# Performance work log

Hardware: AMD Instinct MI355X
Metric: run time of the kernel (lower is better)

## Reference

```python
import jax, jax.numpy as jnp
import numpy as np

B, S, D, H = 32, 2048, 512, 512

def setup_inputs() -> dict:
    key = jax.random.key(0)
    kx, kq, kk, kv = jax.random.split(key, 4)
    scale = 1.0 / np.sqrt(D)
    x = jax.random.normal(kx, (B, S, D), dtype=jnp.float32)
    Wq = jax.random.normal(kq, (D, H), dtype=jnp.float32) * scale
    Wk = jax.random.normal(kk, (D, H), dtype=jnp.float32) * scale
    Wv = jax.random.normal(kv, (D, H), dtype=jnp.float32) * scale
    return {"x": x, "Wq": Wq, "Wk": Wk, "Wv": Wv}

def reference(x, Wq, Wk, Wv):
    # Linear projections (bias=False)
    q = jnp.einsum('bsd,dh->bsh', x, Wq)
    k = jnp.einsum('bsd,dh->bsh', x, Wk)
    v = jnp.einsum('bsd,dh->bsh', x, Wv)
    # Pairwise KL(p_i || q_j) with p = softmax(q_i), q = softmax(k_j):
    #   KL = sum_h p_i log p_i  -  sum_h p_i log q_j
    # The first term is a per-row negative entropy; the second is a GEMM,
    # avoiding the original O(S^2) Python double loop.
    logp = jax.nn.log_softmax(q, axis=-1)          # [B,S,H]
    p = jnp.exp(logp)
    logq = jax.nn.log_softmax(k, axis=-1)          # [B,S,H]
    neg_ent = jnp.sum(p * logp, axis=-1)           # [B,S]
    cross = jnp.einsum('bih,bjh->bij', p, logq)    # [B,S,S]
    kl_divs = neg_ent[:, :, None] - cross          # [B,S,S]
    attn_weights = jax.nn.softmax(-kl_divs, axis=-1)
    attn_output = jnp.einsum('bij,bjh->bih', attn_weights, v)
    return attn_output
```

## Files before the change

kernel.cpp:

```cpp
#include <hip/hip_runtime.h>
#include <hip/hip_bf16.h>

typedef __bf16 bf16x8 __attribute__((ext_vector_type(8)));
typedef float  f32x4  __attribute__((ext_vector_type(4)));

#define NB 32
#define NS 2048
#define ND 512
#define NH 512
#define NROWS (NB*NS)
#define L2E 1.44269504f

__device__ __forceinline__ void gload16(const void* g, void* l) {
  __builtin_amdgcn_global_load_lds((const __attribute__((address_space(1))) void*)g,
                                   (__attribute__((address_space(3))) void*)l, 16, 0, 0);
}

__global__ void prep_w(const float* __restrict__ Wq, const float* __restrict__ Wk,
                       const float* __restrict__ Wv, __bf16* __restrict__ wT) {
  int i = blockIdx.x * blockDim.x + threadIdx.x;
  const int total = 3 * ND * NH;
  for (; i < total; i += gridDim.x * blockDim.x) {
    int m = i / (ND * NH);
    int rem = i - m * (ND * NH);
    int h = rem >> 9;
    int d = rem & 511;
    const float* W = (m == 0) ? Wq : ((m == 1) ? Wk : Wv);
    wT[i] = (__bf16)W[(size_t)d * NH + h];
  }
}

#define K1_XOFF 0
#define K1_WOFF 65536
#define K1_REDM 131072
#define K1_REDS 132096
#define K1_LDS  133120

__global__ __launch_bounds__(512, 2)
void proj_kernel(const float* __restrict__ x, const __bf16* __restrict__ wT,
                 __bf16* __restrict__ p_out, __bf16* __restrict__ k_out,
                 float* __restrict__ L_out, __bf16* __restrict__ vt_out)
{
  __shared__ __align__(16) char smem[K1_LDS];
  char* xb = smem + K1_XOFF;
  char* wb = smem + K1_WOFF;
  float* redm = (float*)(smem + K1_REDM);
  float* reds = (float*)(smem + K1_REDS);

  const int tid = threadIdx.x;
  const int lane = tid & 63, l15 = lane & 15, g = lane >> 4;
  const int w = tid >> 6, rt = w & 1, cs = w >> 1;
  const int r0 = blockIdx.x * 64;
  const int b = r0 >> 11, s0 = r0 & (NS - 1);

  {
    int row = tid >> 3, sc = tid & 7;
    const float* xr = x + (size_t)(r0 + row) * ND;
    #pragma unroll
    for (int u = 0; u < 8; ++u) {
      int s = u * 8 + sc;
      float4 v0 = *(const float4*)(xr + s * 8);
      float4 v1 = *(const float4*)(xr + s * 8 + 4);
      bf16x8 cv;
      cv[0]=(__bf16)v0.x; cv[1]=(__bf16)v0.y; cv[2]=(__bf16)v0.z; cv[3]=(__bf16)v0.w;
      cv[4]=(__bf16)v1.x; cv[5]=(__bf16)v1.y; cv[6]=(__bf16)v1.z; cv[7]=(__bf16)v1.w;
      *(bf16x8*)(xb + row * 1024 + ((s ^ (row & 7)) * 16)) = cv;
    }
  }
  {
    #pragma unroll
    for (int u = 0; u < 4; ++u) {
      int sid = u * 512 + tid, h = sid >> 2, gg = sid & 3;
      gload16(wT + (size_t)h * ND + ((gg ^ ((h >> 1) & 3)) * 8), wb + sid * 16);
    }
  }
  __syncthreads();

  for (int m = 0; m < 3; ++m) {
    f32x4 acc[2][8];
    #pragma unroll
    for (int i2 = 0; i2 < 2; ++i2)
      #pragma unroll
      for (int ht = 0; ht < 8; ++ht) acc[i2][ht] = (f32x4){0.f,0.f,0.f,0.f};

    for (int step = 0; step < 16; ++step) {
      int gs = m * 16 + step;
      char* wcur = wb + (gs & 1) * 32768;
      if (gs + 1 < 48) {
        int gn = gs + 1, mn = gn >> 4, sn = gn & 15;
        const __bf16* wsrc = wT + (size_t)mn * (ND * NH) + sn * 32;
        char* wdst = wb + (gn & 1) * 32768;
        #pragma unroll
        for (int u = 0; u < 4; ++u) {
          int sid = u * 512 + tid, h = sid >> 2, gg = sid & 3;
          gload16(wsrc + (size_t)h * ND + ((gg ^ ((h >> 1) & 3)) * 8), wdst + sid * 16);
        }
      }
      bf16x8 a0, a1;
      {
        int ar = rt * 32 + l15;
        a0 = *(const bf16x8*)(xb + ar * 1024 + (((step * 4 + g) ^ (ar & 7)) * 16));
        ar += 16;
        a1 = *(const bf16x8*)(xb + ar * 1024 + (((step * 4 + g) ^ (ar & 7)) * 16));
      }
      #pragma unroll
      for (int ht = 0; ht < 8; ++ht) {
        int h = cs * 128 + ht * 16 + l15;
        bf16x8 bb = *(const bf16x8*)(wcur + h * 64 + ((g ^ ((h >> 1) & 3)) * 16));
        acc[0][ht] = __builtin_amdgcn_mfma_f32_16x16x32_bf16(a0, bb, acc[0][ht], 0, 0, 0);
        acc[1][ht] = __builtin_amdgcn_mfma_f32_16x16x32_bf16(a1, bb, acc[1][ht], 0, 0, 0);
      }
      __syncthreads();
    }

    if (m == 2) {
      #pragma unroll
      for (int i2 = 0; i2 < 2; ++i2) {
        int sgg = (s0 >> 3) + rt * 4 + i2 * 2 + (g >> 1);
        size_t basep = ((size_t)(b * 256 + sgg)) * 512;
        #pragma unroll
        for (int ht = 0; ht < 8; ++ht) {
          int h = cs * 128 + ht * 16 + l15;
          union { __bf16 h4[4]; ushort4 u4; } cv;
          #pragma unroll
          for (int r = 0; r < 4; ++r) cv.h4[r] = (__bf16)acc[i2][ht][r];
          *(ushort4*)(vt_out + (basep + h) * 8 + (g & 1) * 4) = cv.u4;
        }
      }
    } else {
      float mrow[2][4], tsum[2][4];
      #pragma unroll
      for (int i2 = 0; i2 < 2; ++i2)
        #pragma unroll
        for (int r = 0; r < 4; ++r) {
          float v = acc[i2][0][r];
          #pragma unroll
          for (int ht = 1; ht < 8; ++ht) v = fmaxf(v, acc[i2][ht][r]);
          v = fmaxf(v, __shfl_xor(v, 1)); v = fmaxf(v, __shfl_xor(v, 2));
          v = fmaxf(v, __shfl_xor(v, 4)); v = fmaxf(v, __shfl_xor(v, 8));
          if (l15 == 0) redm[cs * 64 + rt * 32 + i2 * 16 + g * 4 + r] = v;
        }
      __syncthreads();
      #pragma unroll
      for (int i2 = 0; i2 < 2; ++i2)
        #pragma unroll
        for (int r = 0; r < 4; ++r) {
          int row = rt * 32 + i2 * 16 + g * 4 + r;
          mrow[i2][r] = fmaxf(fmaxf(redm[row], redm[64 + row]),
                              fmaxf(redm[128 + row], redm[192 + row]));
        }
      #pragma unroll
      for (int i2 = 0; i2 < 2; ++i2)
        #pragma unroll
        for (int r = 0; r < 4; ++r) {
          float s = 0.f;
          #pragma unroll
          for (int ht = 0; ht < 8; ++ht) s += exp2f((acc[i2][ht][r] - mrow[i2][r]) * L2E);
          s += __shfl_xor(s, 1); s += __shfl_xor(s, 2);
          s += __shfl_xor(s, 4); s += __shfl_xor(s, 8);
          if (l15 == 0) reds[cs * 64 + rt * 32 + i2 * 16 + g * 4 + r] = s;
        }
      __syncthreads();
      #pragma unroll
      for (int i2 = 0; i2 < 2; ++i2)
        #pragma unroll
        for (int r = 0; r < 4; ++r) {
          int row = rt * 32 + i2 * 16 + g * 4 + r;
          tsum[i2][r] = reds[row] + reds[64 + row] + reds[128 + row] + reds[192 + row];
        }
      __bf16* dst = (m == 0) ? p_out : k_out;
      if (m == 0) {
        #pragma unroll
        for (int i2 = 0; i2 < 2; ++i2) {
          float inv[4];
          #pragma unroll
          for (int r = 0; r < 4; ++r) inv[r] = 1.f / tsum[i2][r];
          #pragma unroll
          for (int ht = 0; ht < 8; ++ht) {
            int col = cs * 128 + ht * 16 + l15;
            #pragma unroll
            for (int r = 0; r < 4; ++r) {
              int row = rt * 32 + i2 * 16 + g * 4 + r;
              dst[(size_t)(r0 + row) * NH + col] =
                  (__bf16)(exp2f((acc[i2][ht][r] - mrow[i2][r]) * L2E) * inv[r]);
            }
          }
        }
      } else {
        #pragma unroll
        for (int i2 = 0; i2 < 2; ++i2)
          #pragma unroll
          for (int ht = 0; ht < 8; ++ht) {
            int col = cs * 128 + ht * 16 + l15;
            #pragma unroll
            for (int r = 0; r < 4; ++r) {
              int row = rt * 32 + i2 * 16 + g * 4 + r;
              dst[(size_t)(r0 + row) * NH + col] = (__bf16)acc[i2][ht][r];
            }
          }
        if (cs == 0 && l15 == 0) {
          #pragma unroll
          for (int i2 = 0; i2 < 2; ++i2)
            #pragma unroll
            for (int r = 0; r < 4; ++r) {
              int row = rt * 32 + i2 * 16 + g * 4 + r;
              L_out[r0 + row] = mrow[i2][r] + __logf(tsum[i2][r]);
            }
        }
      }
      __syncthreads();
    }
  }
}

#define QOFF 0
#define KOFF 65536
#define PSTR 512
#define A_LDS 163840

__global__ __launch_bounds__(512, 2)
void attn_kernel(const __bf16* __restrict__ p_all, const __bf16* __restrict__ k_all,
                 const float* __restrict__ L_all, const __bf16* __restrict__ vt_all,
                 float* __restrict__ out)
{
  __shared__ __align__(16) char smem[A_LDS];
  char* Qb = smem + QOFF;
  float* lred = (float*)(smem + KOFF);

  const int bid = blockIdx.x;
  const int b = ((bid >> 8) << 3) + (bid & 7);
  const int ib = (bid >> 3) & 31;
  const int i0 = ib * 64;

  const __bf16* Pg = p_all + (size_t)b * NS * NH;
  const __bf16* Kg = k_all + (size_t)b * NS * NH;
  const float*  Lg = L_all + (size_t)b * NS;
  const __bf16* Vg = vt_all + (size_t)b * (256 * 512 * 8);
  float* Og = out + ((size_t)b * NS + i0) * NH;

  const int tid = threadIdx.x;
  const int lane = tid & 63, l15 = lane & 15, g = lane >> 4;
  const int w = tid >> 6;
  const int ig = w >> 2, jg = w & 3;
  const int hs = w * 64;
  const int xr = l15 & 7;

  #define STAGE(SS) { \
    int j0_ = ((SS) >> 3) * 256, kh_ = (SS) & 7; \
    char* kd_ = smem + KOFF + ((SS) % 3) * 32768; \
    _Pragma("unroll") \
    for (int u_ = 0; u_ < 4; ++u_) { \
      int sid_ = u_ * 512 + tid, jj_ = sid_ >> 3, s8_ = sid_ & 7; \
      gload16(Kg + (size_t)(j0_ + jj_) * NH + kh_ * 64 + ((s8_ ^ (jj_ & 7)) * 8), \
              kd_ + sid_ * 16); \
    } }

  #pragma unroll
  for (int u = 0; u < 8; ++u) {
    int sid = u * 512 + tid, row = sid >> 6, s = sid & 63;
    int sp = (s & 56) | ((s ^ row) & 7);
    gload16(Pg + (size_t)(i0 + row) * NH + sp * 8, Qb + sid * 16);
  }
  STAGE(0);
  STAGE(1);

  f32x4 o_[4][4];
  #pragma unroll
  for (int it = 0; it < 4; ++it)
    #pragma unroll
    for (int ht = 0; ht < 4; ++ht) o_[it][ht] = (f32x4){0.f,0.f,0.f,0.f};
  float lsum[2][4] = {{0.f,0.f,0.f,0.f},{0.f,0.f,0.f,0.f}};

  #define LOADV(DST, JKS) { \
    _Pragma("unroll") \
    for (int ht_ = 0; ht_ < 4; ++ht_) { \
      int h_ = hs + ht_ * 16 + l15; \
      int sg_ = outer * 32 + (JKS) * 4 + g; \
      (DST)[ht_] = *(const bf16x8*)(Vg + ((size_t)sg_ * 512 + h_) * 8); \
    } }
  #define PVSTEP(JKS, VF) { \
    __builtin_amdgcn_s_setprio(1); \
    _Pragma("unroll") \
    for (int it_ = 0; it_ < 4; ++it_) { \
      int row_ = it_ * 16 + l15; \
      int sp_ = ((JKS) * 4 + g) ^ xr; \
      bf16x8 pa_ = *(const bf16x8*)(Pb + row_ * PSTR + sp_ * 16); \
      _Pragma("unroll") \
      for (int ht_ = 0; ht_ < 4; ++ht_) \
        o_[it_][ht_] = __builtin_amdgcn_mfma_f32_16x16x32_bf16(pa_, (VF)[ht_], o_[it_][ht_], 0, 0, 0); \
    } \
    __builtin_amdgcn_s_setprio(0); }

  for (int outer = 0; outer < 8; ++outer) {
    const int j0 = outer * 256;
    f32x4 acc[2][4];
    #pragma unroll
    for (int i2 = 0; i2 < 2; ++i2)
      #pragma unroll
      for (int jt = 0; jt < 4; ++jt) acc[i2][jt] = (f32x4){0.f,0.f,0.f,0.f};

    #pragma unroll
    for (int kk = 0; kk < 8; ++kk) {
      const int ss = outer * 8 + kk;
      asm volatile("s_waitcnt vmcnt(4)" ::: "memory");
      __builtin_amdgcn_sched_barrier(0);
      __builtin_amdgcn_s_barrier();
      __builtin_amdgcn_sched_barrier(0);
      if (ss + 2 < 64) STAGE(ss + 2);
      const char* rb = smem + KOFF + (ss % 3) * 32768;
      #pragma unroll
      for (int sub = 0; sub < 2; ++sub) {
        bf16x8 a0, a1, bq[4];
        {
          int row0 = ig * 32 + l15;
          int seg = kk * 8 + sub * 4 + g;
          a0 = *(const bf16x8*)(Qb + row0 * 1024 + ((seg ^ (row0 & 7)) * 16));
          a1 = *(const bf16x8*)(Qb + (row0 + 16) * 1024 + ((seg ^ ((row0 + 16) & 7)) * 16));
        }
        #pragma unroll
        for (int jt = 0; jt < 4; ++jt) {
          int j = jg * 64 + jt * 16 + l15;
          bq[jt] = *(const bf16x8*)(rb + j * 128 + (((sub * 4 + g) ^ xr) * 16));
        }
        __builtin_amdgcn_s_setprio(1);
        #pragma unroll
        for (int jt = 0; jt < 4; ++jt) {
          acc[0][jt] = __builtin_amdgcn_mfma_f32_16x16x32_bf16(a0, bq[jt], acc[0][jt], 0, 0, 0);
          acc[1][jt] = __builtin_amdgcn_mfma_f32_16x16x32_bf16(a1, bq[jt], acc[1][jt], 0, 0, 0);
        }
        __builtin_amdgcn_s_setprio(0);
      }
    }

    __builtin_amdgcn_sched_barrier(0);
    __builtin_amdgcn_s_barrier();
    __builtin_amdgcn_sched_barrier(0);
    char* Pb = smem + KOFF + ((outer * 8 + 7) % 3) * 32768;

    {
      float LB[4];
      #pragma unroll
      for (int jt = 0; jt < 4; ++jt) LB[jt] = Lg[j0 + jg * 64 + jt * 16 + l15] * L2E;
      #pragma unroll
      for (int i2 = 0; i2 < 2; ++i2)
        #pragma unroll
        for (int jt = 0; jt < 4; ++jt)
          #pragma unroll
          for (int r = 0; r < 4; ++r) {
            float pv = exp2f(acc[i2][jt][r] * L2E - LB[jt]);
            lsum[i2][r] += pv;
            float other = __shfl_xor(pv, 1);
            if ((l15 & 1) == 0) {
              union { __bf16 h; unsigned short u; } lo, hi;
              lo.h = (__bf16)pv; hi.h = (__bf16)other;
              unsigned int pk = (unsigned int)lo.u | ((unsigned int)hi.u << 16);
              int row = ig * 32 + i2 * 16 + g * 4 + r;
              int d = jg * 32 + jt * 8 + (l15 >> 1);
              int s2 = (d >> 2) ^ (row & 7);
              *(unsigned int*)(Pb + row * PSTR + s2 * 16 + (d & 3) * 4) = pk;
            }
          }
    }
    bf16x8 vA[4], vB[4];
    LOADV(vA, 0); LOADV(vB, 1);
    asm volatile("s_waitcnt lgkmcnt(0)" ::: "memory");
    __builtin_amdgcn_sched_barrier(0);
    __builtin_amdgcn_s_barrier();
    __builtin_amdgcn_sched_barrier(0);

    PVSTEP(0, vA); LOADV(vA, 2);
    PVSTEP(1, vB); LOADV(vB, 3);
    PVSTEP(2, vA); LOADV(vA, 4);
    PVSTEP(3, vB); LOADV(vB, 5);
    PVSTEP(4, vA); LOADV(vA, 6);
    PVSTEP(5, vB); LOADV(vB, 7);
    PVSTEP(6, vA);
    PVSTEP(7, vB);
  }

  __syncthreads();
  #pragma unroll
  for (int i2 = 0; i2 < 2; ++i2)
    #pragma unroll
    for (int r = 0; r < 4; ++r) {
      float v = lsum[i2][r];
      v += __shfl_xor(v, 1); v += __shfl_xor(v, 2);
      v += __shfl_xor(v, 4); v += __shfl_xor(v, 8);
      if (l15 == 0) lred[jg * 64 + ig * 32 + i2 * 16 + g * 4 + r] = v;
    }
  __syncthreads();

  #pragma unroll
  for (int it = 0; it < 4; ++it) {
    float inv[4];
    #pragma unroll
    for (int r = 0; r < 4; ++r) {
      int row = it * 16 + g * 4 + r;
      inv[r] = 1.f / (lred[row] + lred[64 + row] + lred[128 + row] + lred[192 + row]);
    }
    #pragma unroll
    for (int ht = 0; ht < 4; ++ht)
      #pragma unroll
      for (int r = 0; r < 4; ++r) {
        int row = it * 16 + g * 4 + r;
        Og[(size_t)row * NH + hs + ht * 16 + l15] = o_[it][ht][r] * inv[r];
      }
  }
}

extern "C" void kernel_launch(void* const* d_in, const int* in_sizes, int n_in,
                              void* d_out, int out_size, void* d_ws, size_t ws_size,
                              hipStream_t stream) {
  const float* x  = (const float*)d_in[0];
  const float* Wq = (const float*)d_in[1];
  const float* Wk = (const float*)d_in[2];
  const float* Wv = (const float*)d_in[3];
  float* out = (float*)d_out;
  char* ws = (char*)d_ws;

  size_t off = 0;
  __bf16* wT   = (__bf16*)(ws + off); off += (size_t)3 * ND * NH * 2;
  __bf16* p_ws = (__bf16*)(ws + off); off += (size_t)NROWS * NH * 2;
  __bf16* k_ws = (__bf16*)(ws + off); off += (size_t)NROWS * NH * 2;
  __bf16* vt_ws= (__bf16*)(ws + off); off += (size_t)NROWS * NH * 2;
  float*  L_ws = (float*)(ws + off);  off += (size_t)NROWS * 4;

  prep_w<<<dim3(512), dim3(256), 0, stream>>>(Wq, Wk, Wv, wT);
  proj_kernel<<<dim3(1024), dim3(512), 0, stream>>>(x, wT, p_ws, k_ws, L_ws, vt_ws);
  attn_kernel<<<dim3(1024), dim3(512), 0, stream>>>(p_ws, k_ws, L_ws, vt_ws, out);
}
```

Before: 660.4 us.

## Split fused attention into scores, row-sum and PV kernels via materialized P

Replaces the single fused attention kernel with three kernels when the workspace is large enough. The first computes exp-shifted scores per 128x128 tile and writes them as bf16 to global memory, along with partial row sums. The second reduces the sums, and the third does a pipelined P·V GEMM with normalization. This decouples the two GEMMs from the online softmax bookkeeping for higher MFMA efficiency, at the cost of writing and reading a large score matrix through HBM.

Result: slower. 735.2 us (+11.3%).

```diff
diff --git a/kernel.cpp b/kernel.cpp
--- a/kernel.cpp
+++ b/kernel.cpp
@@ -211,6 +211,217 @@
       __syncthreads();
     }
   }
+}
+
+__global__ __launch_bounds__(256, 4)
+void scores_kernel(const __bf16* __restrict__ p_all, const __bf16* __restrict__ k_all,
+                   const float* __restrict__ L_all,
+                   __bf16* __restrict__ P_out, float* __restrict__ part_out)
+{
+  __shared__ __align__(16) char smem[65536];
+
+  const int bid = blockIdx.x;
+  const int lb = (bid & 7) * 1024 + (bid >> 3);
+  const int b = lb >> 8, rem = lb & 255, ib = rem >> 4, jb = rem & 15;
+  const int i0 = ib * 128, j0 = jb * 128;
+
+  const __bf16* pg = p_all + (size_t)(b * NS + i0) * NH;
+  const __bf16* kg = k_all + (size_t)(b * NS + j0) * NH;
+  const float*  Lgp = L_all + (size_t)b * NS;
+
+  const int tid = threadIdx.x;
+  const int lane = tid & 63, l15 = lane & 15, g = lane >> 4;
+  const int w = tid >> 6, iw = w >> 1, jw = w & 1;
+
+  #define SC_STAGE(SS) { \
+    char* base_ = smem + ((SS) & 1) * 32768; \
+    _Pragma("unroll") \
+    for (int u_ = 0; u_ < 4; ++u_) { \
+      int sid_ = u_ * 256 + tid, row_ = sid_ >> 3, s8_ = sid_ & 7; \
+      gload16(pg + (size_t)row_ * NH + (SS) * 64 + (((s8_ ^ row_) & 7) * 8), \
+              base_ + sid_ * 16); \
+    } \
+    _Pragma("unroll") \
+    for (int u_ = 0; u_ < 4; ++u_) { \
+      int sid_ = u_ * 256 + tid, row_ = sid_ >> 3, s8_ = sid_ & 7; \
+      gload16(kg + (size_t)row_ * NH + (SS) * 64 + (((s8_ ^ row_) & 7) * 8), \
+              base_ + 16384 + sid_ * 16); \
+    } }
+
+  SC_STAGE(0);
+  __syncthreads();
+
+  f32x4 acc[4][4];
+  #pragma unroll
+  for (int it = 0; it < 4; ++it)
+    #pragma unroll
+    for (int jt = 0; jt < 4; ++jt) acc[it][jt] = (f32x4){0.f,0.f,0.f,0.f};
+
+  for (int ss = 0; ss < 8; ++ss) {
+    const char* Ab = smem + (ss & 1) * 32768;
+    const char* Bb = Ab + 16384;
+    if (ss + 1 < 8) SC_STAGE(ss + 1);
+    #pragma unroll
+    for (int sub = 0; sub < 2; ++sub) {
+      bf16x8 a[4], bq[4];
+      #pragma unroll
+      for (int it = 0; it < 4; ++it) {
+        int row = iw * 64 + it * 16 + l15;
+        a[it] = *(const bf16x8*)(Ab + row * 128 + (((sub * 4 + g) ^ (row & 7)) * 16));
+      }
+      #pragma unroll
+      for (int jt = 0; jt < 4; ++jt) {
+        int row = jw * 64 + jt * 16 + l15;
+        bq[jt] = *(const bf16x8*)(Bb + row * 128 + (((sub * 4 + g) ^ (row & 7)) * 16));
+      }
+      __builtin_amdgcn_s_setprio(1);
+      #pragma unroll
+      for (int it = 0; it < 4; ++it)
+        #pragma unroll
+        for (int jt = 0; jt < 4; ++jt)
+          acc[it][jt] = __builtin_amdgcn_mfma_f32_16x16x32_bf16(a[it], bq[jt], acc[it][jt], 0, 0, 0);
+      __builtin_amdgcn_s_setprio(0);
+    }
+    __syncthreads();
+  }
+
+  float LB[4];
+  #pragma unroll
+  for (int jt = 0; jt < 4; ++jt)
+    LB[jt] = Lgp[j0 + jw * 64 + jt * 16 + l15] * L2E;
+
+  float psum[4][4];
+  #pragma unroll
+  for (int it = 0; it < 4; ++it)
+    #pragma unroll
+    for (int r = 0; r < 4; ++r) psum[it][r] = 0.f;
+
+  #pragma unroll
+  for (int it = 0; it < 4; ++it) {
+    #pragma unroll
+    for (int jt = 0; jt < 4; ++jt) {
+      #pragma unroll
+      for (int r = 0; r < 4; ++r) {
+        float pv = exp2f(acc[it][jt][r] * L2E - LB[jt]);
+        psum[it][r] += pv;
+        float other = __shfl_xor(pv, 1);
+        if ((l15 & 1) == 0) {
+          union { __bf16 h; unsigned short u; } lo, hi;
+          lo.h = (__bf16)pv; hi.h = (__bf16)other;
+          unsigned int pk = (unsigned int)lo.u | ((unsigned int)hi.u << 16);
+          int iabs = i0 + iw * 64 + it * 16 + g * 4 + r;
+          int jabs = j0 + jw * 64 + jt * 16 + l15;
+          *(unsigned int*)((char*)P_out + ((size_t)(b * NS + iabs) * NS + jabs) * 2) = pk;
+        }
+      }
+    }
+  }
+  #pragma unroll
+  for (int it = 0; it < 4; ++it)
+    #pragma unroll
+    for (int r = 0; r < 4; ++r) {
+      float v = psum[it][r];
+      v += __shfl_xor(v, 1); v += __shfl_xor(v, 2);
+      v += __shfl_xor(v, 4); v += __shfl_xor(v, 8);
+      if (l15 == 0)
+        part_out[((size_t)(b * 32 + jb * 2 + jw) << 11) + i0 + iw * 64 + it * 16 + g * 4 + r] = v;
+    }
+}
+
+__global__ void sum_kernel(const float* __restrict__ part, float* __restrict__ linv) {
+  int idx = blockIdx.x * 256 + threadIdx.x;
+  int b = idx >> 11, i = idx & 2047;
+  float s = 0.f;
+  #pragma unroll
+  for (int t = 0; t < 32; ++t) s += part[((size_t)(b * 32 + t) << 11) + i];
+  linv[idx] = 1.f / s;
+}
+
+__global__ __launch_bounds__(512, 2)
+void pv_kernel(const __bf16* __restrict__ P_all, const __bf16* __restrict__ vt_all,
+               const float* __restrict__ linv_all, float* __restrict__ out)
+{
+  __shared__ __align__(16) char smem[73728];
+
+  const int bid = blockIdx.x;
+  const int lb = (bid & 7) * 128 + (bid >> 3);
+  const int b = lb >> 5, rem = lb & 31, ib = rem >> 1, hb = rem & 1;
+  const int i0 = ib * 128, h0 = hb * 256;
+
+  const __bf16* Pg = P_all + (size_t)(b * NS + i0) * NS;
+  const __bf16* Vg = vt_all + (size_t)b * (256 * 512 * 8);
+
+  const int tid = threadIdx.x;
+  const int lane = tid & 63, l15 = lane & 15, g = lane >> 4;
+  const int w = tid >> 6, iw = w >> 2, hw = w & 3;
+
+  #define PV_STAGE(SS) { \
+    char* base_ = smem + ((SS) % 3) * 24576; \
+    { int row_ = tid >> 2, x_ = tid & 3; \
+      gload16(Pg + (size_t)row_ * NS + (SS) * 32 + (((x_ ^ row_) & 3) * 8), \
+              base_ + tid * 16); } \
+    _Pragma("unroll") \
+    for (int u_ = 0; u_ < 2; ++u_) { \
+      int sid_ = u_ * 512 + tid, sl_ = sid_ >> 8, hh_ = sid_ & 255; \
+      gload16(Vg + ((size_t)((SS) * 4 + sl_) * 512 + h0 + hh_) * 8, \
+              base_ + 8192 + sid_ * 16); \
+    } }
+
+  PV_STAGE(0);
+  PV_STAGE(1);
+
+  f32x4 o[4][4];
+  #pragma unroll
+  for (int it = 0; it < 4; ++it)
+    #pragma unroll
+    for (int ht = 0; ht < 4; ++ht) o[it][ht] = (f32x4){0.f,0.f,0.f,0.f};
+
+  for (int ss = 0; ss < 64; ++ss) {
+    if (ss < 63) { asm volatile("s_waitcnt vmcnt(3)" ::: "memory"); }
+    else         { asm volatile("s_waitcnt vmcnt(0)" ::: "memory"); }
+    __builtin_amdgcn_sched_barrier(0);
+    __builtin_amdgcn_s_barrier();
+    __builtin_amdgcn_sched_barrier(0);
+    if (ss + 2 < 64) PV_STAGE(ss + 2);
+
+    const char* Ab = smem + (ss % 3) * 24576;
+    const char* Bb = Ab + 8192;
+    bf16x8 a[4], bq[4];
+    #pragma unroll
+    for (int it = 0; it < 4; ++it) {
+      int row = iw * 64 + it * 16 + l15;
+      a[it] = *(const bf16x8*)(Ab + row * 64 + ((g ^ (row & 3)) * 16));
+    }
+    #pragma unroll
+    for (int ht = 0; ht < 4; ++ht) {
+      int hh = hw * 64 + ht * 16 + l15;
+      bq[ht] = *(const bf16x8*)(Bb + (g * 256 + hh) * 16);
+    }
+    __builtin_amdgcn_s_setprio(1);
+    #pragma unroll
+    for (int it = 0; it < 4; ++it)
+      #pragma unroll
+      for (int ht = 0; ht < 4; ++ht)
+        o[it][ht] = __builtin_amdgcn_mfma_f32_16x16x32_bf16(a[it], bq[ht], o[it][ht], 0, 0, 0);
+    __builtin_amdgcn_s_setprio(0);
+  }
+
+  float linv[4][4];
+  #pragma unroll
+  for (int it = 0; it < 4; ++it)
+    #pragma unroll
+    for (int r = 0; r < 4; ++r)
+      linv[it][r] = linv_all[b * NS + i0 + iw * 64 + it * 16 + g * 4 + r];
+  #pragma unroll
+  for (int it = 0; it < 4; ++it)
+    #pragma unroll
+    for (int ht = 0; ht < 4; ++ht)
+      #pragma unroll
+      for (int r = 0; r < 4; ++r) {
+        int row = i0 + iw * 64 + it * 16 + g * 4 + r;
+        out[((size_t)(b * NS + row)) * NH + h0 + hw * 64 + ht * 16 + l15] =
+            o[it][ht][r] * linv[it][r];
+      }
 }
 
 #define QOFF 0
@@ -424,8 +635,18 @@
   __bf16* k_ws = (__bf16*)(ws + off); off += (size_t)NROWS * NH * 2;
   __bf16* vt_ws= (__bf16*)(ws + off); off += (size_t)NROWS * NH * 2;
   float*  L_ws = (float*)(ws + off);  off += (size_t)NROWS * 4;
+  __bf16* P_ws = (__bf16*)(ws + off); off += (size_t)NB * NS * NS * 2;
+  float*  part = (float*)(ws + off);  off += (size_t)NB * 32 * NS * 4;
+  float*  linv = (float*)(ws + off);  off += (size_t)NROWS * 4;
+  const bool use_split = (ws_size >= off);
 
   prep_w<<<dim3(512), dim3(256), 0, stream>>>(Wq, Wk, Wv, wT);
   proj_kernel<<<dim3(1024), dim3(512), 0, stream>>>(x, wT, p_ws, k_ws, L_ws, vt_ws);
-  attn_kernel<<<dim3(1024), dim3(512), 0, stream>>>(p_ws, k_ws, L_ws, vt_ws, out);
-}
+  if (use_split) {
+    scores_kernel<<<dim3(8192), dim3(256), 0, stream>>>(p_ws, k_ws, L_ws, P_ws, part);
+    sum_kernel<<<dim3(256), dim3(256), 0, stream>>>(part, linv);
+    pv_kernel<<<dim3(1024), dim3(512), 0, stream>>>(P_ws, vt_ws, linv, out);
+  } else {
+    attn_kernel<<<dim3(1024), dim3(512), 0, stream>>>(p_ws, k_ws, L_ws, vt_ws, out);
+  }
+}
```

## Shrink attention LDS footprint: stream P rows from global, halve key tile

Applied to the files above, without the earlier changes.

The attention kernel no longer stages the 64x512 query-probability tile in LDS; each wave reads its A fragments straight from global memory on every k-step. The key tile drops from 256 to 128 columns, K staging goes from triple to double buffering with a full vmcnt(0) wait, and the P scratch tile gets its own region. LDS use falls from 160 KB to 48 KB, so two 512-thread blocks can share a CU and hide latency. The cost is repeated global/L1 traffic for the P rows, less prefetch depth, and twice as many outer iterations with their softmax/PV barriers.

Measured after the change: 1.180 ms. 78.6% more time.

```diff
diff --git a/kernel.cpp b/kernel.cpp
--- a/kernel.cpp
+++ b/kernel.cpp
@@ -213,10 +213,10 @@
   }
 }
 
-#define QOFF 0
-#define KOFF 65536
-#define PSTR 512
-#define A_LDS 163840
+#define SLAB 16384
+#define POFF 32768
+#define PSTR 256
+#define A_LDS 49152
 
 __global__ __launch_bounds__(512, 2)
 void attn_kernel(const __bf16* __restrict__ p_all, const __bf16* __restrict__ k_all,
@@ -224,8 +224,8 @@
                  float* __restrict__ out)
 {
   __shared__ __align__(16) char smem[A_LDS];
-  char* Qb = smem + QOFF;
-  float* lred = (float*)(smem + KOFF);
+  char* Pb = smem + POFF;
+  float* lred = (float*)(smem + POFF);
 
   const int bid = blockIdx.x;
   const int b = ((bid >> 8) << 3) + (bid & 7);
@@ -245,24 +245,20 @@
   const int hs = w * 64;
   const int xr = l15 & 7;
 
+  const __bf16* arow0 = Pg + (size_t)(i0 + ig * 32 + l15) * NH;
+  const __bf16* arow1 = arow0 + 16 * NH;
+
   #define STAGE(SS) { \
-    int j0_ = ((SS) >> 3) * 256, kh_ = (SS) & 7; \
-    char* kd_ = smem + KOFF + ((SS) % 3) * 32768; \
+    int j0_ = ((SS) >> 3) * 128, kh_ = (SS) & 7; \
+    char* kd_ = smem + ((SS) & 1) * SLAB; \
     _Pragma("unroll") \
-    for (int u_ = 0; u_ < 4; ++u_) { \
+    for (int u_ = 0; u_ < 2; ++u_) { \
       int sid_ = u_ * 512 + tid, jj_ = sid_ >> 3, s8_ = sid_ & 7; \
       gload16(Kg + (size_t)(j0_ + jj_) * NH + kh_ * 64 + ((s8_ ^ (jj_ & 7)) * 8), \
               kd_ + sid_ * 16); \
     } }
 
-  #pragma unroll
-  for (int u = 0; u < 8; ++u) {
-    int sid = u * 512 + tid, row = sid >> 6, s = sid & 63;
-    int sp = (s & 56) | ((s ^ row) & 7);
-    gload16(Pg + (size_t)(i0 + row) * NH + sp * 8, Qb + sid * 16);
-  }
   STAGE(0);
-  STAGE(1);
 
   f32x4 o_[4][4];
   #pragma unroll
@@ -271,95 +267,79 @@
     for (int ht = 0; ht < 4; ++ht) o_[it][ht] = (f32x4){0.f,0.f,0.f,0.f};
   float lsum[2][4] = {{0.f,0.f,0.f,0.f},{0.f,0.f,0.f,0.f}};
 
-  #define LOADV(DST, JKS) { \
+  #define LOADV(DST, KS) { \
     _Pragma("unroll") \
     for (int ht_ = 0; ht_ < 4; ++ht_) { \
       int h_ = hs + ht_ * 16 + l15; \
-      int sg_ = outer * 32 + (JKS) * 4 + g; \
+      int sg_ = outer * 16 + (KS) * 4 + g; \
       (DST)[ht_] = *(const bf16x8*)(Vg + ((size_t)sg_ * 512 + h_) * 8); \
     } }
-  #define PVSTEP(JKS, VF) { \
+  #define PVSTEP(KS, VF) { \
     __builtin_amdgcn_s_setprio(1); \
     _Pragma("unroll") \
     for (int it_ = 0; it_ < 4; ++it_) { \
-      int row_ = it_ * 16 + l15; \
-      int sp_ = ((JKS) * 4 + g) ^ xr; \
-      bf16x8 pa_ = *(const bf16x8*)(Pb + row_ * PSTR + sp_ * 16); \
+      bf16x8 pa_ = *(const bf16x8*)(Pb + (it_ * 16 + l15) * PSTR + (((KS) * 4 + g) ^ xr) * 16); \
       _Pragma("unroll") \
       for (int ht_ = 0; ht_ < 4; ++ht_) \
         o_[it_][ht_] = __builtin_amdgcn_mfma_f32_16x16x32_bf16(pa_, (VF)[ht_], o_[it_][ht_], 0, 0, 0); \
     } \
     __builtin_amdgcn_s_setprio(0); }
 
-  for (int outer = 0; outer < 8; ++outer) {
-    const int j0 = outer * 256;
-    f32x4 acc[2][4];
+  for (int outer = 0; outer < 16; ++outer) {
+    const int j0 = outer * 128;
+    f32x4 acc[2][2];
     #pragma unroll
     for (int i2 = 0; i2 < 2; ++i2)
       #pragma unroll
-      for (int jt = 0; jt < 4; ++jt) acc[i2][jt] = (f32x4){0.f,0.f,0.f,0.f};
+      for (int jt = 0; jt < 2; ++jt) acc[i2][jt] = (f32x4){0.f,0.f,0.f,0.f};
 
     #pragma unroll
     for (int kk = 0; kk < 8; ++kk) {
       const int ss = outer * 8 + kk;
-      asm volatile("s_waitcnt vmcnt(4)" ::: "memory");
+      asm volatile("s_waitcnt vmcnt(0)" ::: "memory");
       __builtin_amdgcn_sched_barrier(0);
       __builtin_amdgcn_s_barrier();
       __builtin_amdgcn_sched_barrier(0);
-      if (ss + 2 < 64) STAGE(ss + 2);
-      const char* rb = smem + KOFF + (ss % 3) * 32768;
+
+      const char* rb = smem + (ss & 1) * SLAB;
       #pragma unroll
       for (int sub = 0; sub < 2; ++sub) {
-        bf16x8 a0, a1, bq[4];
-        {
-          int row0 = ig * 32 + l15;
-          int seg = kk * 8 + sub * 4 + g;
-          a0 = *(const bf16x8*)(Qb + row0 * 1024 + ((seg ^ (row0 & 7)) * 16));
-          a1 = *(const bf16x8*)(Qb + (row0 + 16) * 1024 + ((seg ^ ((row0 + 16) & 7)) * 16));
-        }
-        #pragma unroll
-        for (int jt = 0; jt < 4; ++jt) {
-          int j = jg * 64 + jt * 16 + l15;
-          bq[jt] = *(const bf16x8*)(rb + j * 128 + (((sub * 4 + g) ^ xr) * 16));
-        }
+        bf16x8 a0 = *(const bf16x8*)(arow0 + kk * 64 + sub * 32 + g * 8);
+        bf16x8 a1 = *(const bf16x8*)(arow1 + kk * 64 + sub * 32 + g * 8);
+        if (sub == 0) {
+          __builtin_amdgcn_sched_barrier(0);
+          if (ss + 1 < 128) STAGE(ss + 1);
+        }
+        bf16x8 b0 = *(const bf16x8*)(rb + (jg * 32 + l15) * 128 + (((sub * 4 + g) ^ xr) * 16));
+        bf16x8 b1 = *(const bf16x8*)(rb + (jg * 32 + 16 + l15) * 128 + (((sub * 4 + g) ^ xr) * 16));
         __builtin_amdgcn_s_setprio(1);
-        #pragma unroll
-        for (int jt = 0; jt < 4; ++jt) {
-          acc[0][jt] = __builtin_amdgcn_mfma_f32_16x16x32_bf16(a0, bq[jt], acc[0][jt], 0, 0, 0);
-          acc[1][jt] = __builtin_amdgcn_mfma_f32_16x16x32_bf16(a1, bq[jt], acc[1][jt], 0, 0, 0);
-        }
+        acc[0][0] = __builtin_amdgcn_mfma_f32_16x16x32_bf16(a0, b0, acc[0][0], 0, 0, 0);
+        acc[1][0] = __builtin_amdgcn_mfma_f32_16x16x32_bf16(a1, b0, acc[1][0], 0, 0, 0);
+        acc[0][1] = __builtin_amdgcn_mfma_f32_16x16x32_bf16(a0, b1, acc[0][1], 0, 0, 0);
+        acc[1][1] = __builtin_amdgcn_mfma_f32_16x16x32_bf16(a1, b1, acc[1][1], 0, 0, 0);
         __builtin_amdgcn_s_setprio(0);
       }
     }
 
-    __builtin_amdgcn_sched_barrier(0);
-    __builtin_amdgcn_s_barrier();
-    __builtin_amdgcn_sched_barrier(0);
-    char* Pb = smem + KOFF + ((outer * 8 + 7) % 3) * 32768;
-
-    {
-      float LB[4];
-      #pragma unroll
-      for (int jt = 0; jt < 4; ++jt) LB[jt] = Lg[j0 + jg * 64 + jt * 16 + l15] * L2E;
+    #pragma unroll
+    for (int jt = 0; jt < 2; ++jt) {
+      float LB = Lg[j0 + jg * 32 + jt * 16 + l15] * L2E;
       #pragma unroll
       for (int i2 = 0; i2 < 2; ++i2)
         #pragma unroll
-        for (int jt = 0; jt < 4; ++jt)
-          #pragma unroll
-          for (int r = 0; r < 4; ++r) {
-            float pv = exp2f(acc[i2][jt][r] * L2E - LB[jt]);
-            lsum[i2][r] += pv;
-            float other = __shfl_xor(pv, 1);
-            if ((l15 & 1) == 0) {
-              union { __bf16 h; unsigned short u; } lo, hi;
-              lo.h = (__bf16)pv; hi.h = (__bf16)other;
-              unsigned int pk = (unsigned int)lo.u | ((unsigned int)hi.u << 16);
-              int row = ig * 32 + i2 * 16 + g * 4 + r;
-              int d = jg * 32 + jt * 8 + (l15 >> 1);
-              int s2 = (d >> 2) ^ (row & 7);
-              *(unsigned int*)(Pb + row * PSTR + s2 * 16 + (d & 3) * 4) = pk;
-            }
+        for (int r = 0; r < 4; ++r) {
+          float pv = exp2f(acc[i2][jt][r] * L2E - LB);
+          lsum[i2][r] += pv;
+          float other = __shfl_xor(pv, 1);
+          if ((l15 & 1) == 0) {
+            union { __bf16 h; unsigned short u; } lo, hi;
+            lo.h = (__bf16)pv; hi.h = (__bf16)other;
+            unsigned int pk = (unsigned int)lo.u | ((unsigned int)hi.u << 16);
+            int row = ig * 32 + i2 * 16 + g * 4 + r;
+            int d = jg * 16 + jt * 8 + (l15 >> 1);
+            *(unsigned int*)(Pb + row * PSTR + ((d >> 2) ^ (row & 7)) * 16 + (d & 3) * 4) = pk;
           }
+        }
     }
     bf16x8 vA[4], vB[4];
     LOADV(vA, 0); LOADV(vB, 1);
@@ -370,12 +350,8 @@
 
     PVSTEP(0, vA); LOADV(vA, 2);
     PVSTEP(1, vB); LOADV(vB, 3);
-    PVSTEP(2, vA); LOADV(vA, 4);
-    PVSTEP(3, vB); LOADV(vB, 5);
-    PVSTEP(4, vA); LOADV(vA, 6);
-    PVSTEP(5, vB); LOADV(vB, 7);
-    PVSTEP(6, vA);
-    PVSTEP(7, vB);
+    PVSTEP(2, vA);
+    PVSTEP(3, vB);
   }
 
   __syncthreads();
```

## Give each wave a private K slice to drop per-stage block barriers

Applied to the files above, without the earlier changes.

Each of the 8 waves now loads its own 32-row slice of the K tile into a private region of the LDS stage buffer and computes the QK tile for all 64 query rows against only those key rows. Because a wave consumes only data it loaded itself, the block-wide barrier inside each k-step becomes a per-wave vmcnt wait, leaving only a barrier at the softmax/PV boundary and one at the end of each outer iteration. This cuts block synchronisation in the QK loop. In exchange, Q fragments are re-read from LDS by every wave (4 A-loads per 4 MFMAs instead of sharing), row-sum partials grow to 8 per row, and lsum register use rises.

Measured after the change: 759.9 us. 15.1% more time.

```diff
diff --git a/kernel.cpp b/kernel.cpp
--- a/kernel.cpp
+++ b/kernel.cpp
@@ -241,18 +241,18 @@
   const int tid = threadIdx.x;
   const int lane = tid & 63, l15 = lane & 15, g = lane >> 4;
   const int w = tid >> 6;
-  const int ig = w >> 2, jg = w & 3;
   const int hs = w * 64;
   const int xr = l15 & 7;
 
   #define STAGE(SS) { \
     int j0_ = ((SS) >> 3) * 256, kh_ = (SS) & 7; \
-    char* kd_ = smem + KOFF + ((SS) % 3) * 32768; \
+    char* kd_ = smem + KOFF + ((SS) % 3) * 32768 + w * 4096; \
     _Pragma("unroll") \
     for (int u_ = 0; u_ < 4; ++u_) { \
-      int sid_ = u_ * 512 + tid, jj_ = sid_ >> 3, s8_ = sid_ & 7; \
-      gload16(Kg + (size_t)(j0_ + jj_) * NH + kh_ * 64 + ((s8_ ^ (jj_ & 7)) * 8), \
-              kd_ + sid_ * 16); \
+      int unit_ = u_ * 64 + lane; \
+      int jl_ = unit_ >> 3, s8_ = unit_ & 7; \
+      gload16(Kg + (size_t)(j0_ + w * 32 + jl_) * NH + kh_ * 64 + ((s8_ ^ (jl_ & 7)) * 8), \
+              kd_ + unit_ * 16); \
     } }
 
   #pragma unroll
@@ -263,28 +263,34 @@
   }
   STAGE(0);
   STAGE(1);
+  asm volatile("s_waitcnt vmcnt(4)" ::: "memory");
+  __builtin_amdgcn_sched_barrier(0);
+  __builtin_amdgcn_s_barrier();
+  __builtin_amdgcn_sched_barrier(0);
 
   f32x4 o_[4][4];
   #pragma unroll
   for (int it = 0; it < 4; ++it)
     #pragma unroll
     for (int ht = 0; ht < 4; ++ht) o_[it][ht] = (f32x4){0.f,0.f,0.f,0.f};
-  float lsum[2][4] = {{0.f,0.f,0.f,0.f},{0.f,0.f,0.f,0.f}};
-
-  #define LOADV(DST, JKS) { \
+  float lsum[4][4];
+  #pragma unroll
+  for (int it = 0; it < 4; ++it)
+    #pragma unroll
+    for (int r = 0; r < 4; ++r) lsum[it][r] = 0.f;
+
+  #define LOADV(DST, KS) { \
     _Pragma("unroll") \
     for (int ht_ = 0; ht_ < 4; ++ht_) { \
       int h_ = hs + ht_ * 16 + l15; \
-      int sg_ = outer * 32 + (JKS) * 4 + g; \
+      int sg_ = outer * 32 + (KS) * 4 + g; \
       (DST)[ht_] = *(const bf16x8*)(Vg + ((size_t)sg_ * 512 + h_) * 8); \
     } }
-  #define PVSTEP(JKS, VF) { \
+  #define PVSTEP(KS, VF) { \
     __builtin_amdgcn_s_setprio(1); \
     _Pragma("unroll") \
     for (int it_ = 0; it_ < 4; ++it_) { \
-      int row_ = it_ * 16 + l15; \
-      int sp_ = ((JKS) * 4 + g) ^ xr; \
-      bf16x8 pa_ = *(const bf16x8*)(Pb + row_ * PSTR + sp_ * 16); \
+      bf16x8 pa_ = *(const bf16x8*)(Pb + (it_ * 16 + l15) * PSTR + (((KS) * 4 + g) ^ xr) * 16); \
       _Pragma("unroll") \
       for (int ht_ = 0; ht_ < 4; ++ht_) \
         o_[it_][ht_] = __builtin_amdgcn_mfma_f32_16x16x32_bf16(pa_, (VF)[ht_], o_[it_][ht_], 0, 0, 0); \
@@ -293,42 +299,43 @@
 
   for (int outer = 0; outer < 8; ++outer) {
     const int j0 = outer * 256;
-    f32x4 acc[2][4];
-    #pragma unroll
-    for (int i2 = 0; i2 < 2; ++i2)
-      #pragma unroll
-      for (int jt = 0; jt < 4; ++jt) acc[i2][jt] = (f32x4){0.f,0.f,0.f,0.f};
+    f32x4 acc[4][2];
+    #pragma unroll
+    for (int it = 0; it < 4; ++it)
+      #pragma unroll
+      for (int jt = 0; jt < 2; ++jt) acc[it][jt] = (f32x4){0.f,0.f,0.f,0.f};
 
     #pragma unroll
     for (int kk = 0; kk < 8; ++kk) {
       const int ss = outer * 8 + kk;
-      asm volatile("s_waitcnt vmcnt(4)" ::: "memory");
-      __builtin_amdgcn_sched_barrier(0);
-      __builtin_amdgcn_s_barrier();
+      if (ss < 63) { asm volatile("s_waitcnt vmcnt(4)" ::: "memory"); }
+      else         { asm volatile("s_waitcnt vmcnt(0)" ::: "memory"); }
       __builtin_amdgcn_sched_barrier(0);
       if (ss + 2 < 64) STAGE(ss + 2);
       const char* rb = smem + KOFF + (ss % 3) * 32768;
       #pragma unroll
       for (int sub = 0; sub < 2; ++sub) {
-        bf16x8 a0, a1, bq[4];
+        bf16x8 b0, b1;
         {
-          int row0 = ig * 32 + l15;
-          int seg = kk * 8 + sub * 4 + g;
-          a0 = *(const bf16x8*)(Qb + row0 * 1024 + ((seg ^ (row0 & 7)) * 16));
-          a1 = *(const bf16x8*)(Qb + (row0 + 16) * 1024 + ((seg ^ ((row0 + 16) & 7)) * 16));
-        }
-        #pragma unroll
-        for (int jt = 0; jt < 4; ++jt) {
-          int j = jg * 64 + jt * 16 + l15;
-          bq[jt] = *(const bf16x8*)(rb + j * 128 + (((sub * 4 + g) ^ xr) * 16));
-        }
-        __builtin_amdgcn_s_setprio(1);
-        #pragma unroll
-        for (int jt = 0; jt < 4; ++jt) {
-          acc[0][jt] = __builtin_amdgcn_mfma_f32_16x16x32_bf16(a0, bq[jt], acc[0][jt], 0, 0, 0);
-          acc[1][jt] = __builtin_amdgcn_mfma_f32_16x16x32_bf16(a1, bq[jt], acc[1][jt], 0, 0, 0);
-        }
-        __builtin_amdgcn_s_setprio(0);
+          int jr = w * 32 + l15;
+          b0 = *(const bf16x8*)(rb + jr * 128 + (((sub * 4 + g) ^ xr) * 16));
+          b1 = *(const bf16x8*)(rb + (jr + 16) * 128 + (((sub * 4 + g) ^ xr) * 16));
+        }
+        #pragma unroll
+        for (int ith = 0; ith < 2; ++ith) {
+          bf16x8 a0, a1;
+          int r0w = ith * 32 + l15;
+          a0 = *(const bf16x8*)(Qb + r0w * 1024 +
+                (((kk * 8 + sub * 4 + g) ^ (r0w & 7)) * 16));
+          a1 = *(const bf16x8*)(Qb + (r0w + 16) * 1024 +
+                (((kk * 8 + sub * 4 + g) ^ ((r0w + 16) & 7)) * 16));
+          __builtin_amdgcn_s_setprio(1);
+          acc[ith*2  ][0] = __builtin_amdgcn_mfma_f32_16x16x32_bf16(a0, b0, acc[ith*2  ][0], 0, 0, 0);
+          acc[ith*2  ][1] = __builtin_amdgcn_mfma_f32_16x16x32_bf16(a0, b1, acc[ith*2  ][1], 0, 0, 0);
+          acc[ith*2+1][0] = __builtin_amdgcn_mfma_f32_16x16x32_bf16(a1, b0, acc[ith*2+1][0], 0, 0, 0);
+          acc[ith*2+1][1] = __builtin_amdgcn_mfma_f32_16x16x32_bf16(a1, b1, acc[ith*2+1][1], 0, 0, 0);
+          __builtin_amdgcn_s_setprio(0);
+        }
       }
     }
 
@@ -338,26 +345,25 @@
     char* Pb = smem + KOFF + ((outer * 8 + 7) % 3) * 32768;
 
     {
-      float LB[4];
-      #pragma unroll
-      for (int jt = 0; jt < 4; ++jt) LB[jt] = Lg[j0 + jg * 64 + jt * 16 + l15] * L2E;
-      #pragma unroll
-      for (int i2 = 0; i2 < 2; ++i2)
-        #pragma unroll
-        for (int jt = 0; jt < 4; ++jt)
+      float LB[2];
+      LB[0] = Lg[j0 + w * 32 + l15] * L2E;
+      LB[1] = Lg[j0 + w * 32 + 16 + l15] * L2E;
+      #pragma unroll
+      for (int it = 0; it < 4; ++it)
+        #pragma unroll
+        for (int jt = 0; jt < 2; ++jt)
           #pragma unroll
           for (int r = 0; r < 4; ++r) {
-            float pv = exp2f(acc[i2][jt][r] * L2E - LB[jt]);
-            lsum[i2][r] += pv;
+            float pv = exp2f(acc[it][jt][r] * L2E - LB[jt]);
+            lsum[it][r] += pv;
             float other = __shfl_xor(pv, 1);
             if ((l15 & 1) == 0) {
               union { __bf16 h; unsigned short u; } lo, hi;
               lo.h = (__bf16)pv; hi.h = (__bf16)other;
               unsigned int pk = (unsigned int)lo.u | ((unsigned int)hi.u << 16);
-              int row = ig * 32 + i2 * 16 + g * 4 + r;
-              int d = jg * 32 + jt * 8 + (l15 >> 1);
-              int s2 = (d >> 2) ^ (row & 7);
-              *(unsigned int*)(Pb + row * PSTR + s2 * 16 + (d & 3) * 4) = pk;
+              int row = it * 16 + g * 4 + r;
+              int d = w * 16 + jt * 8 + (l15 >> 1);
+              *(unsigned int*)(Pb + row * PSTR + ((d >> 2) ^ (row & 7)) * 16 + (d & 3) * 4) = pk;
             }
           }
     }
@@ -376,17 +382,21 @@
     PVSTEP(5, vB); LOADV(vB, 7);
     PVSTEP(6, vA);
     PVSTEP(7, vB);
+
+    __builtin_amdgcn_sched_barrier(0);
+    __builtin_amdgcn_s_barrier();
+    __builtin_amdgcn_sched_barrier(0);
   }
 
   __syncthreads();
   #pragma unroll
-  for (int i2 = 0; i2 < 2; ++i2)
+  for (int it = 0; it < 4; ++it)
     #pragma unroll
     for (int r = 0; r < 4; ++r) {
-      float v = lsum[i2][r];
+      float v = lsum[it][r];
       v += __shfl_xor(v, 1); v += __shfl_xor(v, 2);
       v += __shfl_xor(v, 4); v += __shfl_xor(v, 8);
-      if (l15 == 0) lred[jg * 64 + ig * 32 + i2 * 16 + g * 4 + r] = v;
+      if (l15 == 0) lred[w * 64 + it * 16 + g * 4 + r] = v;
     }
   __syncthreads();
 
@@ -396,7 +406,10 @@
     #pragma unroll
     for (int r = 0; r < 4; ++r) {
       int row = it * 16 + g * 4 + r;
-      inv[r] = 1.f / (lred[row] + lred[64 + row] + lred[128 + row] + lred[192 + row]);
+      float s = 0.f;
+      #pragma unroll
+      for (int ww = 0; ww < 8; ++ww) s += lred[ww * 64 + row];
+      inv[r] = 1.f / s;
     }
     #pragma unroll
     for (int ht = 0; ht < 4; ++ht)
```
